# Optimization experiments

Measured on AMD Instinct MI355X. Metric: run time of the kernel, lower is better.

Reference implementation:

```python
import jax, jax.numpy as jnp
import numpy as np

S, D, H = 4096, 2048, 16
HD = D // H

def setup_inputs() -> dict:
    key = jax.random.key(0)
    ks = jax.random.split(key, 9)
    s = 1.0 / np.sqrt(D)
    return {
        "hidden_states": jax.random.normal(ks[0], (S, D), jnp.float32),
        "Wq": jax.random.uniform(ks[1], (D, D), jnp.float32, -s, s),
        "bq": jax.random.uniform(ks[2], (D,), jnp.float32, -s, s),
        "Wk": jax.random.uniform(ks[3], (D, D), jnp.float32, -s, s),
        "bk": jax.random.uniform(ks[4], (D,), jnp.float32, -s, s),
        "Wv": jax.random.uniform(ks[5], (D, D), jnp.float32, -s, s),
        "bv": jax.random.uniform(ks[6], (D,), jnp.float32, -s, s),
        "Wo": jax.random.uniform(ks[7], (D, D), jnp.float32, -s, s),
        "bo": jax.random.uniform(ks[8], (D,), jnp.float32, -s, s),
    }

def reference(hidden_states, Wq, bq, Wk, bk, Wv, bv, Wo, bo):
    seq = hidden_states.shape[0]
    # projections (torch Linear: x @ W.T + b)
    q = (hidden_states @ Wq.T + bq).reshape(seq, H, HD).transpose(1, 0, 2)  # [H,S,hd]
    k = (hidden_states @ Wk.T + bk).reshape(seq, H, HD).transpose(1, 0, 2)
    v = (hidden_states @ Wv.T + bv).reshape(seq, H, HD).transpose(1, 0, 2)
    scale = 1.0 / np.sqrt(HD).astype(np.float32)
    qk = jnp.einsum('hqd,hkd->hqk', q, k) * scale  # [H,S,S]
    causal = jnp.tril(jnp.ones((seq, seq), bool))
    qk = jnp.where(causal, qk, -jnp.inf)
    attn = jax.nn.softmax(qk, axis=-1)
    out = jnp.einsum('hqk,hkd->hqd', attn, v)  # [H,S,hd]
    out = out.transpose(1, 0, 2).reshape(seq, D)
    return out @ Wo.T + bo
```

## Files before the change

kernel.cpp:

```cpp
#include <hip/hip_runtime.h>
#include <stdint.h>

#define S_LEN 4096
#define D_DIM 2048
#define NHEAD 16
#define HDIM  128

typedef short bf16x8 __attribute__((ext_vector_type(8)));
typedef float f32x4  __attribute__((ext_vector_type(4)));
typedef float f32x16 __attribute__((ext_vector_type(16)));

__device__ __forceinline__ unsigned short f2bf(float x) {
  union { float f; unsigned u; } v; v.f = x;
  unsigned r = v.u + 0x7FFFu + ((v.u >> 16) & 1u);
  return (unsigned short)(r >> 16);
}

__device__ __forceinline__ float bf2f(unsigned short s) {
  union { unsigned u; float f; } v; v.u = ((unsigned)s) << 16;
  return v.f;
}

__device__ __forceinline__ unsigned cvtpk_bf16(float lo, float hi_) {
  unsigned r;
  asm("v_cvt_pk_bf16_f32 %0, %1, %2" : "=v"(r) : "v"(lo), "v"(hi_));
  return r;
}

__device__ __forceinline__ void gload_lds16(const void* g, void* l) {
  __builtin_amdgcn_global_load_lds(
      (const __attribute__((address_space(1))) unsigned int*)g,
      (__attribute__((address_space(3))) unsigned int*)l, 16, 0, 0);
}

__global__ __launch_bounds__(256) void cvt_all(
    const float* __restrict__ X, const float* __restrict__ Wq,
    const float* __restrict__ Wk, const float* __restrict__ Wv,
    const float* __restrict__ Wo, unsigned short* __restrict__ out) {
  const size_t DD = (size_t)D_DIM * D_DIM;
  size_t i = ((size_t)blockIdx.x * 256 + threadIdx.x) * 8;
  const float* src; size_t off;
  if (i < 2 * DD)      { src = X;  off = i; }
  else if (i < 3 * DD) { src = Wq; off = i - 2 * DD; }
  else if (i < 4 * DD) { src = Wk; off = i - 3 * DD; }
  else if (i < 5 * DD) { src = Wv; off = i - 4 * DD; }
  else                 { src = Wo; off = i - 5 * DD; }
  float4 a = *(const float4*)(src + off);
  float4 b = *(const float4*)(src + off + 4);
  union { unsigned short s[8]; bf16x8 v; } o;
  o.s[0] = f2bf(a.x); o.s[1] = f2bf(a.y); o.s[2] = f2bf(a.z); o.s[3] = f2bf(a.w);
  o.s[4] = f2bf(b.x); o.s[5] = f2bf(b.y); o.s[6] = f2bf(b.z); o.s[7] = f2bf(b.w);
  *(bf16x8*)(out + i) = o.v;
}

template<bool OUT_BF16>
__global__ __launch_bounds__(256, 2) void gemm_bt(
    const unsigned short* __restrict__ A, const unsigned short* __restrict__ B,
    const float* __restrict__ bias, void* __restrict__ Cout,
    int M, int N, int K, float esc) {
  __shared__ __attribute__((aligned(16))) unsigned short As[128 * 32];
  __shared__ __attribute__((aligned(16))) unsigned short Bs[128 * 32];
  const int m0 = blockIdx.y * 128, n0 = blockIdx.x * 128;
  const int tid = threadIdx.x, lane = tid & 63, wv = tid >> 6;
  const int wm = wv >> 1, wn = wv & 1;
  const int rA = lane & 15, kb = (lane >> 4) * 8;

  f32x4 acc[4][4];
#pragma unroll
  for (int i = 0; i < 4; ++i)
#pragma unroll
    for (int j = 0; j < 4; ++j)
#pragma unroll
      for (int r = 0; r < 4; ++r) acc[i][j][r] = 0.f;

  for (int k0 = 0; k0 < K; k0 += 32) {
    __syncthreads();
#pragma unroll
    for (int p = 0; p < 2; ++p) {
      const int rr = (wv * 2 + p) * 16 + (lane >> 2);
      const int cc = lane & 3;
      gload_lds16(A + (size_t)(m0 + rr) * K + k0 + cc * 8, As + (wv * 2 + p) * 512);
      gload_lds16(B + (size_t)(n0 + rr) * K + k0 + cc * 8, Bs + (wv * 2 + p) * 512);
    }
    __syncthreads();
    bf16x8 af[4], bfr[4];
#pragma unroll
    for (int i = 0; i < 4; ++i)
      af[i] = *(const bf16x8*)(As + (wm * 64 + i * 16 + rA) * 32 + kb);
#pragma unroll
    for (int j = 0; j < 4; ++j)
      bfr[j] = *(const bf16x8*)(Bs + (wn * 64 + j * 16 + rA) * 32 + kb);
#pragma unroll
    for (int i = 0; i < 4; ++i)
#pragma unroll
      for (int j = 0; j < 4; ++j)
        acc[i][j] = __builtin_amdgcn_mfma_f32_16x16x32_bf16(af[i], bfr[j], acc[i][j], 0, 0, 0);
  }

  const int cR = (lane >> 4) * 4, cC = lane & 15;
#pragma unroll
  for (int j = 0; j < 4; ++j) {
    const int col = n0 + wn * 64 + j * 16 + cC;
    const float bv = bias[col];
#pragma unroll
    for (int i = 0; i < 4; ++i) {
      const int row0 = m0 + wm * 64 + i * 16 + cR;
#pragma unroll
      for (int r = 0; r < 4; ++r) {
        const float v = (acc[i][j][r] + bv) * esc;
        if (OUT_BF16)
          ((unsigned short*)Cout)[(size_t)(row0 + r) * N + col] = f2bf(v);
        else
          ((float*)Cout)[(size_t)(row0 + r) * N + col] = v;
      }
    }
  }
}

__global__ __launch_bounds__(256, 2) void attn_part(
    const unsigned short* __restrict__ Qb, const unsigned short* __restrict__ Kb,
    const unsigned short* __restrict__ Vb, unsigned short* __restrict__ Opart,
    float* __restrict__ ML) {
  __shared__ __attribute__((aligned(16))) unsigned short Ks[64 * 128];
  __shared__ __attribute__((aligned(16))) unsigned short Vt[128 * 64];
  const int bid = blockIdx.x;
  const int h  = ((bid & 7) << 1) | ((bid >> 3) & 1);
  const int hf = (bid >> 4) & 1;
  const int qi = 31 - (bid >> 5);
  const int q0 = qi * 128;
  const int u2 = (h * 32 + qi) * 2 + hf;
  const int tid = threadIdx.x, lane = tid & 63, wv = tid >> 6;
  const int qc = lane & 31, hi = lane >> 5;
  const int q0w = q0 + wv * 32;
  const int myq = q0w + qc;
  const int kp = tid & 31, hb = (tid >> 5) * 16;

  bf16x8 qf[8];
#pragma unroll
  for (int sl = 0; sl < 8; ++sl)
    qf[sl] = *(const bf16x8*)(Qb + (size_t)myq * D_DIM + h * HDIM + sl * 16 + hi * 8);

  f32x16 oacc[4];
#pragma unroll
  for (int nf = 0; nf < 4; ++nf)
#pragma unroll
    for (int r = 0; r < 16; ++r) oacc[nf][r] = 0.f;
  float mh = -3.0e38f, l = 0.f;

  const int klo = hf * (qi + 1), khi = klo + qi + 1;
  const int wqmax = q0w + 31;

  for (int kt = klo; kt < khi; ++kt) {
    const int k0 = kt * 64;
    __syncthreads();
#pragma unroll
    for (int p = 0; p < 4; ++p) {
      const int ob = wv * 4096 + p * 1024;
      const int o = ob + lane * 16;
      const int r = o >> 8, c = (o >> 4) & 15;
      gload_lds16(Kb + (size_t)(k0 + r) * D_DIM + h * HDIM + (c ^ (r & 7)) * 8,
                  Ks + ob / 2);
    }
    {
      const unsigned short* s0 = Vb + (size_t)(k0 + 2 * kp) * D_DIM + h * HDIM + hb;
      union { uint4 u[4]; unsigned short s[32]; } t;
      t.u[0] = *(const uint4*)s0;           t.u[1] = *(const uint4*)(s0 + 8);
      t.u[2] = *(const uint4*)(s0 + D_DIM); t.u[3] = *(const uint4*)(s0 + D_DIM + 8);
#pragma unroll
      for (int w = 0; w < 16; ++w) {
        const int hd = hb + w;
        const unsigned val = (unsigned)t.s[w] | ((unsigned)t.s[16 + w] << 16);
        *(unsigned*)((char*)Vt + hd * 128 + (((kp >> 2) ^ (hd & 7)) << 4) + ((kp & 3) << 2)) = val;
      }
    }
    __syncthreads();
    if (k0 > wqmax) continue;

    f32x16 sacc[2];
#pragma unroll
    for (int kb = 0; kb < 2; ++kb)
#pragma unroll
      for (int r = 0; r < 16; ++r) sacc[kb][r] = 0.f;
    __builtin_amdgcn_s_setprio(1);
#pragma unroll
    for (int sl = 0; sl < 8; ++sl) {
#pragma unroll
      for (int kb = 0; kb < 2; ++kb) {
        const int row = kb * 32 + qc;
        bf16x8 kfr = *(const bf16x8*)((const char*)Ks + row * 256 +
                                      (((2 * sl + hi) ^ (qc & 7)) << 4));
        sacc[kb] = __builtin_amdgcn_mfma_f32_32x32x16_bf16(kfr, qf[sl], sacc[kb], 0, 0, 0);
      }
    }
    __builtin_amdgcn_s_setprio(0);

    const bool needmask = (k0 + 63 > q0w);
    if (needmask) {
      const int dq = myq - k0;
#pragma unroll
      for (int kb = 0; kb < 2; ++kb)
#pragma unroll
        for (int r = 0; r < 16; ++r) {
          const int kk = kb * 32 + (r & 3) + 8 * (r >> 2) + 4 * hi;
          if (kk > dq) sacc[kb][r] = -3.0e38f;
        }
    }
    float mx0[8];
#pragma unroll
    for (int t = 0; t < 8; ++t)
      mx0[t] = fmaxf(fmaxf(sacc[0][t], sacc[0][t + 8]),
                     fmaxf(sacc[1][t], sacc[1][t + 8]));
    float mx = fmaxf(fmaxf(fmaxf(mx0[0], mx0[1]), fmaxf(mx0[2], mx0[3])),
                     fmaxf(fmaxf(mx0[4], mx0[5]), fmaxf(mx0[6], mx0[7])));
    mx = fmaxf(mx, __shfl_xor(mx, 32));
    if (!__all(mx <= mh + 11.5f)) {
      const float mnew = fmaxf(mh, mx);
      const float corr = exp2f(mh - mnew);
      mh = mnew;
      l *= corr;
#pragma unroll
      for (int r = 0; r < 16; ++r) {
        const float cr = __shfl(corr, (r & 3) + 8 * (r >> 2) + 4 * hi);
#pragma unroll
        for (int nf = 0; nf < 4; ++nf) oacc[nf][r] *= cr;
      }
    }
    float rs = 0.f;
#pragma unroll
    for (int kb = 0; kb < 2; ++kb)
#pragma unroll
      for (int r = 0; r < 16; ++r) {
        const float p = exp2f(sacc[kb][r] - mh);
        sacc[kb][r] = p;
        rs += p;
      }
    rs += __shfl_xor(rs, 32);
    l += rs;

    bf16x8 pa[4];
#pragma unroll
    for (int kb = 0; kb < 2; ++kb)
#pragma unroll
      for (int s = 0; s < 2; ++s) {
        const int b = s * 8;
        unsigned pk0 = cvtpk_bf16(sacc[kb][b + 0], sacc[kb][b + 1]);
        unsigned pk1 = cvtpk_bf16(sacc[kb][b + 2], sacc[kb][b + 3]);
        unsigned pk2 = cvtpk_bf16(sacc[kb][b + 4], sacc[kb][b + 5]);
        unsigned pk3 = cvtpk_bf16(sacc[kb][b + 6], sacc[kb][b + 7]);
        const unsigned sw0 = (unsigned)__shfl_xor((int)pk0, 32);
        const unsigned sw1 = (unsigned)__shfl_xor((int)pk1, 32);
        const unsigned sw2 = (unsigned)__shfl_xor((int)pk2, 32);
        const unsigned sw3 = (unsigned)__shfl_xor((int)pk3, 32);
        union { unsigned u[4]; bf16x8 v; } f;
        if (hi) { f.u[0] = sw2; f.u[1] = sw3; f.u[2] = pk2; f.u[3] = pk3; }
        else    { f.u[0] = pk0; f.u[1] = pk1; f.u[2] = sw0; f.u[3] = sw1; }
        pa[kb * 2 + s] = f.v;
      }

    __builtin_amdgcn_s_setprio(1);
#pragma unroll
    for (int nf = 0; nf < 4; ++nf) {
      const int hd = 32 * nf + qc;
#pragma unroll
      for (int ks = 0; ks < 4; ++ks) {
        bf16x8 vf = *(const bf16x8*)((const char*)Vt + hd * 128 +
                                     (((2 * ks + hi) ^ (qc & 7)) << 4));
        oacc[nf] = __builtin_amdgcn_mfma_f32_32x32x16_bf16(pa[ks], vf, oacc[nf], 0, 0, 0);
      }
    }
    __builtin_amdgcn_s_setprio(0);
  }

  unsigned short* ob = Opart + (size_t)u2 * 16384;
#pragma unroll
  for (int r = 0; r < 16; ++r) {
    const int rl = wv * 32 + (r & 3) + 8 * (r >> 2) + 4 * hi;
#pragma unroll
    for (int nf = 0; nf < 4; ++nf)
      ob[rl * 128 + 32 * nf + qc] = f2bf(oacc[nf][r]);
  }
  if (hi == 0) {
    ML[(size_t)u2 * 256 + wv * 32 + qc] = mh;
    ML[(size_t)u2 * 256 + 128 + wv * 32 + qc] = l;
  }
}

__global__ __launch_bounds__(256) void attn_combine(
    const unsigned short* __restrict__ Opart, const float* __restrict__ ML,
    unsigned short* __restrict__ Ob) {
  const int u = blockIdx.x;
  const int h = u >> 5, qi = u & 31;
  const int tid = threadIdx.x;
  const int row = tid >> 1, c0 = (tid & 1) * 64;
  const float m1 = ML[(size_t)(u * 2 + 0) * 256 + row];
  const float l1 = ML[(size_t)(u * 2 + 0) * 256 + 128 + row];
  const float m2 = ML[(size_t)(u * 2 + 1) * 256 + row];
  const float l2 = ML[(size_t)(u * 2 + 1) * 256 + 128 + row];
  const float M  = fmaxf(m1, m2);
  const float a1 = exp2f(m1 - M), a2 = exp2f(m2 - M);
  const float inv = 1.f / (a1 * l1 + a2 * l2);
  const unsigned short* p1 = Opart + (size_t)(u * 2 + 0) * 16384 + row * 128 + c0;
  const unsigned short* p2 = Opart + (size_t)(u * 2 + 1) * 16384 + row * 128 + c0;
  unsigned short* o = Ob + (size_t)(qi * 128 + row) * D_DIM + h * HDIM + c0;
#pragma unroll
  for (int c = 0; c < 64; c += 8) {
    bf16x8 v1 = *(const bf16x8*)(p1 + c);
    bf16x8 v2 = *(const bf16x8*)(p2 + c);
    union { unsigned short s[8]; bf16x8 v; } out;
#pragma unroll
    for (int e = 0; e < 8; ++e)
      out.s[e] = f2bf((bf2f((unsigned short)v1[e]) * a1 +
                       bf2f((unsigned short)v2[e]) * a2) * inv);
    *(bf16x8*)(o + c) = out.v;
  }
}

extern "C" void kernel_launch(void* const* d_in, const int* in_sizes, int n_in,
                              void* d_out, int out_size, void* d_ws, size_t ws_size,
                              hipStream_t stream) {
  const float* X  = (const float*)d_in[0];
  const float* Wq = (const float*)d_in[1];
  const float* bq = (const float*)d_in[2];
  const float* Wk = (const float*)d_in[3];
  const float* bk = (const float*)d_in[4];
  const float* Wv = (const float*)d_in[5];
  const float* bv = (const float*)d_in[6];
  const float* Wo = (const float*)d_in[7];
  const float* bo = (const float*)d_in[8];
  float* out = (float*)d_out;

  unsigned short* ws = (unsigned short*)d_ws;
  const size_t SD = (size_t)S_LEN * D_DIM;
  const size_t DD = (size_t)D_DIM * D_DIM;
  unsigned short* Xb  = ws;
  unsigned short* Wqb = Xb + SD;
  unsigned short* Wkb = Wqb + DD;
  unsigned short* Wvb = Wkb + DD;
  unsigned short* Wob = Wvb + DD;
  unsigned short* Qb  = Wob + DD;
  unsigned short* Kb  = Qb + SD;
  unsigned short* Vb  = Kb + SD;
  unsigned short* AOb = Vb + SD;
  unsigned short* Opart = ws;
  float* ML = (float*)(ws + SD + 2 * DD);

  cvt_all<<<(int)(6 * DD / 8 / 256), 256, 0, stream>>>(X, Wq, Wk, Wv, Wo, Xb);

  const float qsc = 0.08838834764831845f * 1.4426950408889634f;
  dim3 gg(D_DIM / 128, S_LEN / 128);
  gemm_bt<true><<<gg, 256, 0, stream>>>(Xb, Wqb, bq, Qb, S_LEN, D_DIM, D_DIM, qsc);
  gemm_bt<true><<<gg, 256, 0, stream>>>(Xb, Wkb, bk, Kb, S_LEN, D_DIM, D_DIM, 1.0f);
  gemm_bt<true><<<gg, 256, 0, stream>>>(Xb, Wvb, bv, Vb, S_LEN, D_DIM, D_DIM, 1.0f);

  attn_part<<<dim3(1024), 256, 0, stream>>>(Qb, Kb, Vb, Opart, ML);
  attn_combine<<<dim3(512), 256, 0, stream>>>(Opart, ML, AOb);

  gemm_bt<false><<<gg, 256, 0, stream>>>(AOb, Wob, bo, out, S_LEN, D_DIM, D_DIM, 1.0f);
}
```

Baseline: 348.9 us.

## Fuse QKV projections into one GEMM and enlarge attention blocks to 256 queries

The three Q/K/V projection GEMMs become a single launch over the concatenated weight matrix, with the epilogue routing each column segment to its own bias, output and scale. The attention kernel moves to 512-thread blocks covering 256 queries each, so every loaded K/V tile is shared by eight waves instead of four. Its work order is also remapped with a serpentine schedule across XCDs for balance. The combine kernel is rewritten to match the new partition layout. The aim is fewer launches, better GEMM wave fill, and less K/V reload traffic, at the cost of larger blocks that may limit occupancy.

```diff
diff --git a/kernel.cpp b/kernel.cpp
--- a/kernel.cpp
+++ b/kernel.cpp
@@ -53,17 +53,81 @@
   *(bf16x8*)(out + i) = o.v;
 }
 
-template<bool OUT_BF16>
-__global__ __launch_bounds__(256, 2) void gemm_bt(
-    const unsigned short* __restrict__ A, const unsigned short* __restrict__ B,
-    const float* __restrict__ bias, void* __restrict__ Cout,
-    int M, int N, int K, float esc) {
+__global__ __launch_bounds__(256, 2) void gemm_qkv(
+    const unsigned short* __restrict__ A, const unsigned short* __restrict__ W,
+    const float* __restrict__ bq, const float* __restrict__ bk,
+    const float* __restrict__ bv, unsigned short* __restrict__ Q,
+    unsigned short* __restrict__ Ko, unsigned short* __restrict__ V,
+    float qsc) {
   __shared__ __attribute__((aligned(16))) unsigned short As[128 * 32];
   __shared__ __attribute__((aligned(16))) unsigned short Bs[128 * 32];
   const int m0 = blockIdx.y * 128, n0 = blockIdx.x * 128;
   const int tid = threadIdx.x, lane = tid & 63, wv = tid >> 6;
   const int wm = wv >> 1, wn = wv & 1;
   const int rA = lane & 15, kb = (lane >> 4) * 8;
+  const int K = D_DIM;
+
+  f32x4 acc[4][4];
+#pragma unroll
+  for (int i = 0; i < 4; ++i)
+#pragma unroll
+    for (int j = 0; j < 4; ++j)
+#pragma unroll
+      for (int r = 0; r < 4; ++r) acc[i][j][r] = 0.f;
+
+  for (int k0 = 0; k0 < K; k0 += 32) {
+    __syncthreads();
+#pragma unroll
+    for (int p = 0; p < 2; ++p) {
+      const int rr = (wv * 2 + p) * 16 + (lane >> 2);
+      const int cc = lane & 3;
+      gload_lds16(A + (size_t)(m0 + rr) * K + k0 + cc * 8, As + (wv * 2 + p) * 512);
+      gload_lds16(W + (size_t)(n0 + rr) * K + k0 + cc * 8, Bs + (wv * 2 + p) * 512);
+    }
+    __syncthreads();
+    bf16x8 af[4], bfr[4];
+#pragma unroll
+    for (int i = 0; i < 4; ++i)
+      af[i] = *(const bf16x8*)(As + (wm * 64 + i * 16 + rA) * 32 + kb);
+#pragma unroll
+    for (int j = 0; j < 4; ++j)
+      bfr[j] = *(const bf16x8*)(Bs + (wn * 64 + j * 16 + rA) * 32 + kb);
+#pragma unroll
+    for (int i = 0; i < 4; ++i)
+#pragma unroll
+      for (int j = 0; j < 4; ++j)
+        acc[i][j] = __builtin_amdgcn_mfma_f32_16x16x32_bf16(af[i], bfr[j], acc[i][j], 0, 0, 0);
+  }
+
+  const int cR = (lane >> 4) * 4, cC = lane & 15;
+#pragma unroll
+  for (int j = 0; j < 4; ++j) {
+    const int col = n0 + wn * 64 + j * 16 + cC;
+    const int seg = col >> 11, cl = col & 2047;
+    const float* bp = (seg == 0) ? bq : (seg == 1) ? bk : bv;
+    unsigned short* op = (seg == 0) ? Q : (seg == 1) ? Ko : V;
+    const float es = (seg == 0) ? qsc : 1.0f;
+    const float bvv = bp[cl];
+#pragma unroll
+    for (int i = 0; i < 4; ++i) {
+      const int row0 = m0 + wm * 64 + i * 16 + cR;
+#pragma unroll
+      for (int r = 0; r < 4; ++r)
+        op[(size_t)(row0 + r) * D_DIM + cl] = f2bf((acc[i][j][r] + bvv) * es);
+    }
+  }
+}
+
+__global__ __launch_bounds__(256, 2) void gemm_bt_f32(
+    const unsigned short* __restrict__ A, const unsigned short* __restrict__ B,
+    const float* __restrict__ bias, float* __restrict__ Cout,
+    int M, int N, int K) {
+  __shared__ __attribute__((aligned(16))) unsigned short As[128 * 32];
+  __shared__ __attribute__((aligned(16))) unsigned short Bs[128 * 32];
+  const int m0 = blockIdx.y * 128, n0 = blockIdx.x * 128;
+  const int tid = threadIdx.x, lane = tid & 63, wv = tid >> 6;
+  const int wm = wv >> 1, wn = wv & 1;
+  const int rA = lane & 15, kb = (lane >> 4) * 8;
 
   f32x4 acc[4][4];
 #pragma unroll
@@ -101,39 +165,36 @@
 #pragma unroll
   for (int j = 0; j < 4; ++j) {
     const int col = n0 + wn * 64 + j * 16 + cC;
-    const float bv = bias[col];
+    const float bvv = bias[col];
 #pragma unroll
     for (int i = 0; i < 4; ++i) {
       const int row0 = m0 + wm * 64 + i * 16 + cR;
 #pragma unroll
-      for (int r = 0; r < 4; ++r) {
-        const float v = (acc[i][j][r] + bv) * esc;
-        if (OUT_BF16)
-          ((unsigned short*)Cout)[(size_t)(row0 + r) * N + col] = f2bf(v);
-        else
-          ((float*)Cout)[(size_t)(row0 + r) * N + col] = v;
-      }
-    }
-  }
-}
-
-__global__ __launch_bounds__(256, 2) void attn_part(
+      for (int r = 0; r < 4; ++r)
+        Cout[(size_t)(row0 + r) * N + col] = acc[i][j][r] + bvv;
+    }
+  }
+}
+
+__global__ __launch_bounds__(512, 4) void attn_part(
     const unsigned short* __restrict__ Qb, const unsigned short* __restrict__ Kb,
     const unsigned short* __restrict__ Vb, unsigned short* __restrict__ Opart,
     float* __restrict__ ML) {
   __shared__ __attribute__((aligned(16))) unsigned short Ks[64 * 128];
   __shared__ __attribute__((aligned(16))) unsigned short Vt[128 * 64];
   const int bid = blockIdx.x;
-  const int h  = ((bid & 7) << 1) | ((bid >> 3) & 1);
-  const int hf = (bid >> 4) & 1;
-  const int qi = 31 - (bid >> 5);
-  const int q0 = qi * 128;
-  const int u2 = (h * 32 + qi) * 2 + hf;
+  const int xcd = bid & 7, rb = bid >> 3;
+  const int d = (rb < 32) ? rb : 95 - rb;
+  const int qp = 15 - (d >> 2);
+  const int h = (xcd << 1) | (d & 1);
+  const int hf = (d >> 1) & 1;
+  const int q0 = qp * 256;
+  const int u2 = (h * 16 + qp) * 2 + hf;
   const int tid = threadIdx.x, lane = tid & 63, wv = tid >> 6;
   const int qc = lane & 31, hi = lane >> 5;
   const int q0w = q0 + wv * 32;
   const int myq = q0w + qc;
-  const int kp = tid & 31, hb = (tid >> 5) * 16;
+  const int kp = tid & 31, hb = (tid >> 5) * 8;
 
   bf16x8 qf[8];
 #pragma unroll
@@ -147,15 +208,16 @@
     for (int r = 0; r < 16; ++r) oacc[nf][r] = 0.f;
   float mh = -3.0e38f, l = 0.f;
 
-  const int klo = hf * (qi + 1), khi = klo + qi + 1;
+  const int ntil = 2 * (qp + 1);
+  const int klo = hf * ntil, khi = klo + ntil;
   const int wqmax = q0w + 31;
 
   for (int kt = klo; kt < khi; ++kt) {
     const int k0 = kt * 64;
     __syncthreads();
 #pragma unroll
-    for (int p = 0; p < 4; ++p) {
-      const int ob = wv * 4096 + p * 1024;
+    for (int p = 0; p < 2; ++p) {
+      const int ob = wv * 2048 + p * 1024;
       const int o = ob + lane * 16;
       const int r = o >> 8, c = (o >> 4) & 15;
       gload_lds16(Kb + (size_t)(k0 + r) * D_DIM + h * HDIM + (c ^ (r & 7)) * 8,
@@ -163,13 +225,13 @@
     }
     {
       const unsigned short* s0 = Vb + (size_t)(k0 + 2 * kp) * D_DIM + h * HDIM + hb;
-      union { uint4 u[4]; unsigned short s[32]; } t;
-      t.u[0] = *(const uint4*)s0;           t.u[1] = *(const uint4*)(s0 + 8);
-      t.u[2] = *(const uint4*)(s0 + D_DIM); t.u[3] = *(const uint4*)(s0 + D_DIM + 8);
-#pragma unroll
-      for (int w = 0; w < 16; ++w) {
+      union { uint4 u[2]; unsigned short s[16]; } t;
+      t.u[0] = *(const uint4*)s0;
+      t.u[1] = *(const uint4*)(s0 + D_DIM);
+#pragma unroll
+      for (int w = 0; w < 8; ++w) {
         const int hd = hb + w;
-        const unsigned val = (unsigned)t.s[w] | ((unsigned)t.s[16 + w] << 16);
+        const unsigned val = (unsigned)t.s[w] | ((unsigned)t.s[8 + w] << 16);
         *(unsigned*)((char*)Vt + hd * 128 + (((kp >> 2) ^ (hd & 7)) << 4) + ((kp & 3) << 2)) = val;
       }
     }
@@ -271,7 +333,7 @@
     __builtin_amdgcn_s_setprio(0);
   }
 
-  unsigned short* ob = Opart + (size_t)u2 * 16384;
+  unsigned short* ob = Opart + (size_t)u2 * 32768;
 #pragma unroll
   for (int r = 0; r < 16; ++r) {
     const int rl = wv * 32 + (r & 3) + 8 * (r >> 2) + 4 * hi;
@@ -280,8 +342,8 @@
       ob[rl * 128 + 32 * nf + qc] = f2bf(oacc[nf][r]);
   }
   if (hi == 0) {
-    ML[(size_t)u2 * 256 + wv * 32 + qc] = mh;
-    ML[(size_t)u2 * 256 + 128 + wv * 32 + qc] = l;
+    ML[(size_t)u2 * 512 + wv * 32 + qc] = mh;
+    ML[(size_t)u2 * 512 + 256 + wv * 32 + qc] = l;
   }
 }
 
@@ -289,29 +351,29 @@
     const unsigned short* __restrict__ Opart, const float* __restrict__ ML,
     unsigned short* __restrict__ Ob) {
   const int u = blockIdx.x;
-  const int h = u >> 5, qi = u & 31;
+  const int h = u >> 4, qp = u & 15;
   const int tid = threadIdx.x;
-  const int row = tid >> 1, c0 = (tid & 1) * 64;
-  const float m1 = ML[(size_t)(u * 2 + 0) * 256 + row];
-  const float l1 = ML[(size_t)(u * 2 + 0) * 256 + 128 + row];
-  const float m2 = ML[(size_t)(u * 2 + 1) * 256 + row];
-  const float l2 = ML[(size_t)(u * 2 + 1) * 256 + 128 + row];
-  const float M  = fmaxf(m1, m2);
-  const float a1 = exp2f(m1 - M), a2 = exp2f(m2 - M);
-  const float inv = 1.f / (a1 * l1 + a2 * l2);
-  const unsigned short* p1 = Opart + (size_t)(u * 2 + 0) * 16384 + row * 128 + c0;
-  const unsigned short* p2 = Opart + (size_t)(u * 2 + 1) * 16384 + row * 128 + c0;
-  unsigned short* o = Ob + (size_t)(qi * 128 + row) * D_DIM + h * HDIM + c0;
-#pragma unroll
-  for (int c = 0; c < 64; c += 8) {
-    bf16x8 v1 = *(const bf16x8*)(p1 + c);
-    bf16x8 v2 = *(const bf16x8*)(p2 + c);
-    union { unsigned short s[8]; bf16x8 v; } out;
+  const unsigned short* p1 = Opart + (size_t)(u * 2 + 0) * 32768;
+  const unsigned short* p2 = Opart + (size_t)(u * 2 + 1) * 32768;
+  const float* ml1 = ML + (size_t)(u * 2 + 0) * 512;
+  const float* ml2 = ML + (size_t)(u * 2 + 1) * 512;
+#pragma unroll
+  for (int i = 0; i < 16; ++i) {
+    const int chunk = i * 256 + tid;
+    const int row = chunk >> 4, col = (chunk & 15) * 8;
+    const float m1 = ml1[row], l1 = ml1[256 + row];
+    const float m2 = ml2[row], l2 = ml2[256 + row];
+    const float M = fmaxf(m1, m2);
+    const float a1 = exp2f(m1 - M), a2 = exp2f(m2 - M);
+    const float inv = 1.f / (a1 * l1 + a2 * l2);
+    bf16x8 v1 = *(const bf16x8*)(p1 + chunk * 8);
+    bf16x8 v2 = *(const bf16x8*)(p2 + chunk * 8);
+    union { unsigned short s[8]; bf16x8 v; } o;
 #pragma unroll
     for (int e = 0; e < 8; ++e)
-      out.s[e] = f2bf((bf2f((unsigned short)v1[e]) * a1 +
-                       bf2f((unsigned short)v2[e]) * a2) * inv);
-    *(bf16x8*)(o + c) = out.v;
+      o.s[e] = f2bf((bf2f((unsigned short)v1[e]) * a1 +
+                     bf2f((unsigned short)v2[e]) * a2) * inv);
+    *(bf16x8*)(Ob + (size_t)(qp * 256 + row) * D_DIM + h * HDIM + col) = o.v;
   }
 }
 
@@ -334,9 +396,7 @@
   const size_t DD = (size_t)D_DIM * D_DIM;
   unsigned short* Xb  = ws;
   unsigned short* Wqb = Xb + SD;
-  unsigned short* Wkb = Wqb + DD;
-  unsigned short* Wvb = Wkb + DD;
-  unsigned short* Wob = Wvb + DD;
+  unsigned short* Wob = Wqb + 3 * DD;
   unsigned short* Qb  = Wob + DD;
   unsigned short* Kb  = Qb + SD;
   unsigned short* Vb  = Kb + SD;
@@ -347,13 +407,10 @@
   cvt_all<<<(int)(6 * DD / 8 / 256), 256, 0, stream>>>(X, Wq, Wk, Wv, Wo, Xb);
 
   const float qsc = 0.08838834764831845f * 1.4426950408889634f;
-  dim3 gg(D_DIM / 128, S_LEN / 128);
-  gemm_bt<true><<<gg, 256, 0, stream>>>(Xb, Wqb, bq, Qb, S_LEN, D_DIM, D_DIM, qsc);
-  gemm_bt<true><<<gg, 256, 0, stream>>>(Xb, Wkb, bk, Kb, S_LEN, D_DIM, D_DIM, 1.0f);
-  gemm_bt<true><<<gg, 256, 0, stream>>>(Xb, Wvb, bv, Vb, S_LEN, D_DIM, D_DIM, 1.0f);
-
-  attn_part<<<dim3(1024), 256, 0, stream>>>(Qb, Kb, Vb, Opart, ML);
-  attn_combine<<<dim3(512), 256, 0, stream>>>(Opart, ML, AOb);
-
-  gemm_bt<false><<<gg, 256, 0, stream>>>(AOb, Wob, bo, out, S_LEN, D_DIM, D_DIM, 1.0f);
-}
+  gemm_qkv<<<dim3(48, 32), 256, 0, stream>>>(Xb, Wqb, bq, bk, bv, Qb, Kb, Vb, qsc);
+
+  attn_part<<<dim3(512), 512, 0, stream>>>(Qb, Kb, Vb, Opart, ML);
+  attn_combine<<<dim3(256), 256, 0, stream>>>(Opart, ML, AOb);
+
+  gemm_bt_f32<<<dim3(16, 32), 256, 0, stream>>>(AOb, Wob, bo, out, S_LEN, D_DIM, D_DIM);
+}
```

Result: slower. 548.6 us (+57.2%).
